# Kernel optimization log

Measured on AMD Instinct MI355X. Metric: run time of the kernel, lower is better.

## Reference

```python
import jax, jax.numpy as jnp
import numpy as np

ALPHA = 1.0  # self.alpha_ in ClusterNet


def setup_inputs() -> dict:
    key = jax.random.key(0)
    k1, k2 = jax.random.split(key)
    z = jax.random.normal(k1, (8192, 256), dtype=jnp.float32)
    centroids = jax.random.normal(k2, (64, 256), dtype=jnp.float32)
    return {"z": z, "centroids": centroids}


def reference(z, centroids):
    # similarity='EUC': pairwise euclidean distance (bs, n_clusters)
    diff = z[:, None, :] - centroids[None, :, :]          # (bs, K, H)
    sim = jnp.sqrt(jnp.sum(diff * diff, axis=2))          # (bs, K)
    # Student-t soft assignment, alpha = 1 -> Q = (1 + sim)^-1
    Q = jnp.power(1.0 + sim / ALPHA, -(ALPHA + 1.0) / 2.0)
    Q = Q / jnp.sum(Q, axis=1, keepdims=True)             # row-normalize
    # Target distribution P
    P = jnp.square(Q) / jnp.sum(Q, axis=0, keepdims=True)  # col-sum of Q
    P = P / jnp.sum(P, axis=1, keepdims=True)              # row-normalize
    return (Q, P)
```

## Files before the change

### kernel.cpp

```cpp
#include <hip/hip_runtime.h>


#define M  8192
#define NC 64
#define H  256
#define BM 64
#define BK 64
#define LDT 68

__global__ __launch_bounds__(256) void k1_dist_partial(
    const float* __restrict__ Z, const float* __restrict__ C,
    float* __restrict__ out)
{
    __shared__ float Zt[BK][LDT];
    __shared__ float Ct[BK][LDT];
    const int t  = threadIdx.x;
    const int bx = blockIdx.x;
    const int m0 = (bx >> 1) * BM;
    const int khalf = bx & 1;
    const int tx = t & 15, ty = t >> 4;
    const int kl = (t & 15) * 4;
    const int ml = t >> 4;

    float acc[4][4] = {};

    for (int chunk = 0; chunk < 2; ++chunk) {
        const int kb = khalf * 128 + chunk * BK;
        #pragma unroll
        for (int s = 0; s < 4; ++s) {
            const int m = ml + 16 * s;
            float4 v = *(const float4*)&Z[(m0 + m) * H + kb + kl];
            Zt[kl + 0][m] = v.x; Zt[kl + 1][m] = v.y;
            Zt[kl + 2][m] = v.z; Zt[kl + 3][m] = v.w;
            float4 w = *(const float4*)&C[m * H + kb + kl];
            Ct[kl + 0][m] = w.x; Ct[kl + 1][m] = w.y;
            Ct[kl + 2][m] = w.z; Ct[kl + 3][m] = w.w;
        }
        __syncthreads();
        #pragma unroll 8
        for (int kk = 0; kk < BK; ++kk) {
            float4 a4 = *(const float4*)&Zt[kk][ty * 4];
            float4 b4 = *(const float4*)&Ct[kk][tx * 4];
            float ar[4] = {a4.x, a4.y, a4.z, a4.w};
            float br[4] = {b4.x, b4.y, b4.z, b4.w};
            #pragma unroll
            for (int r = 0; r < 4; ++r)
                #pragma unroll
                for (int c = 0; c < 4; ++c) {
                    float d = ar[r] - br[c];
                    acc[r][c] += d * d;
                }
        }
        __syncthreads();
    }

    float* dst = out + (size_t)khalf * (M * NC);
    #pragma unroll
    for (int r = 0; r < 4; ++r) {
        float4 v = make_float4(acc[r][0], acc[r][1], acc[r][2], acc[r][3]);
        *(float4*)&dst[(m0 + ty * 4 + r) * NC + tx * 4] = v;
    }
}

__global__ void k0_zero(float* __restrict__ colsum) {
    colsum[threadIdx.x] = 0.0f;
}

__global__ __launch_bounds__(256) void k2_q(
    float* __restrict__ out, float* __restrict__ colsum)
{
    __shared__ float cs[NC];
    const int t = threadIdx.x;
    if (t < NC) cs[t] = 0.0f;
    __syncthreads();
    const int lane = t & 63;
    const int wid  = t >> 6;
    const int rowBase = blockIdx.x * 32;
    float local = 0.0f;
    for (int it = 0; it < 8; ++it) {
        const int row = rowBase + it * 4 + wid;
        float p0 = out[row * NC + lane];
        float p1 = out[(size_t)M * NC + row * NC + lane];
        float d  = sqrtf(p0 + p1);
        float q  = 1.0f / (1.0f + d);
        float s = q;
        #pragma unroll
        for (int m = 1; m < 64; m <<= 1) s += __shfl_xor(s, m);
        float Q = q / s;
        out[row * NC + lane] = Q;
        local += Q;
    }
    atomicAdd(&cs[lane], local);
    __syncthreads();
    if (t < NC) atomicAdd(&colsum[t], cs[t]);
}

__global__ __launch_bounds__(256) void k3_p(
    float* __restrict__ out, const float* __restrict__ colsum)
{
    const int t = threadIdx.x;
    const int lane = t & 63;
    const int wid  = t >> 6;
    const float invcs = 1.0f / colsum[lane];
    const int rowBase = blockIdx.x * 32;
    for (int it = 0; it < 8; ++it) {
        const int row = rowBase + it * 4 + wid;
        float q  = out[row * NC + lane];
        float pr = q * q * invcs;
        float s = pr;
        #pragma unroll
        for (int m = 1; m < 64; m <<= 1) s += __shfl_xor(s, m);
        out[(size_t)M * NC + row * NC + lane] = pr / s;
    }
}

extern "C" void kernel_launch(void* const* d_in, const int* in_sizes, int n_in,
                              void* d_out, int out_size, void* d_ws, size_t ws_size,
                              hipStream_t stream) {
    const float* Z = (const float*)d_in[0];
    const float* C = (const float*)d_in[1];
    float* out = (float*)d_out;
    float* colsum = (float*)d_ws;

    k0_zero<<<1, NC, 0, stream>>>(colsum);
    k1_dist_partial<<<256, 256, 0, stream>>>(Z, C, out);
    k2_q<<<256, 256, 0, stream>>>(out, colsum);
    k3_p<<<256, 256, 0, stream>>>(out, colsum);
}
```

Before: 89.91 us.

## Fuse distance and Q computation via norm expansion, drop atomics and extra launches

```diff
diff --git a/kernel.cpp b/kernel.cpp
--- a/kernel.cpp
+++ b/kernel.cpp
@@ -4,113 +4,149 @@
 #define M  8192
 #define NC 64
 #define H  256
-#define BM 64
-#define BK 64
-#define LDT 68
+#define BM 32
 
-__global__ __launch_bounds__(256) void k1_dist_partial(
+__global__ __launch_bounds__(256, 1) void k1_fused(
     const float* __restrict__ Z, const float* __restrict__ C,
-    float* __restrict__ out)
+    float* __restrict__ out, float* __restrict__ ws)
 {
-    __shared__ float Zt[BK][LDT];
-    __shared__ float Ct[BK][LDT];
-    const int t  = threadIdx.x;
-    const int bx = blockIdx.x;
-    const int m0 = (bx >> 1) * BM;
-    const int khalf = bx & 1;
-    const int tx = t & 15, ty = t >> 4;
-    const int kl = (t & 15) * 4;
-    const int ml = t >> 4;
+    __shared__ float pd[4][BM][NC];
+    __shared__ float ncp[4][NC];
+    __shared__ float nzs[BM];
+    __shared__ float csum[4][NC];
 
-    float acc[4][4] = {};
+    const int t    = threadIdx.x;
+    const int lane = t & 63;
+    const int wid  = __builtin_amdgcn_readfirstlane(t >> 6);
+    const int row0 = blockIdx.x * BM;
 
-    for (int chunk = 0; chunk < 2; ++chunk) {
-        const int kb = khalf * 128 + chunk * BK;
+    {
+        const int r  = t >> 3;
+        const int sg = t & 7;
+        const float4* zr = (const float4*)(Z + (size_t)(row0 + r) * H);
+        float s = 0.f;
         #pragma unroll
-        for (int s = 0; s < 4; ++s) {
-            const int m = ml + 16 * s;
-            float4 v = *(const float4*)&Z[(m0 + m) * H + kb + kl];
-            Zt[kl + 0][m] = v.x; Zt[kl + 1][m] = v.y;
-            Zt[kl + 2][m] = v.z; Zt[kl + 3][m] = v.w;
-            float4 w = *(const float4*)&C[m * H + kb + kl];
-            Ct[kl + 0][m] = w.x; Ct[kl + 1][m] = w.y;
-            Ct[kl + 2][m] = w.z; Ct[kl + 3][m] = w.w;
+        for (int i = 0; i < 8; ++i) {
+            float4 v = zr[sg * 8 + i];
+            s += v.x * v.x + v.y * v.y + v.z * v.z + v.w * v.w;
         }
-        __syncthreads();
-        #pragma unroll 8
-        for (int kk = 0; kk < BK; ++kk) {
-            float4 a4 = *(const float4*)&Zt[kk][ty * 4];
-            float4 b4 = *(const float4*)&Ct[kk][tx * 4];
-            float ar[4] = {a4.x, a4.y, a4.z, a4.w};
-            float br[4] = {b4.x, b4.y, b4.z, b4.w};
-            #pragma unroll
-            for (int r = 0; r < 4; ++r)
-                #pragma unroll
-                for (int c = 0; c < 4; ++c) {
-                    float d = ar[r] - br[c];
-                    acc[r][c] += d * d;
-                }
-        }
-        __syncthreads();
+        s += __shfl_xor(s, 1);
+        s += __shfl_xor(s, 2);
+        s += __shfl_xor(s, 4);
+        if (sg == 0) nzs[r] = s;
     }
 
-    float* dst = out + (size_t)khalf * (M * NC);
+    float4 c4[16];
+    {
+        const float4* cp = (const float4*)(C + (size_t)lane * H + wid * 64);
+        #pragma unroll
+        for (int i = 0; i < 16; ++i) c4[i] = cp[i];
+    }
+    {
+        float s = 0.f;
+        #pragma unroll
+        for (int i = 0; i < 16; ++i)
+            s += c4[i].x * c4[i].x + c4[i].y * c4[i].y + c4[i].z * c4[i].z + c4[i].w * c4[i].w;
+        ncp[wid][lane] = s;
+    }
+
+    float acc[BM];
     #pragma unroll
-    for (int r = 0; r < 4; ++r) {
-        float4 v = make_float4(acc[r][0], acc[r][1], acc[r][2], acc[r][3]);
-        *(float4*)&dst[(m0 + ty * 4 + r) * NC + tx * 4] = v;
+    for (int r = 0; r < BM; ++r) acc[r] = 0.f;
+
+    const float* Zb = Z + (size_t)row0 * H + wid * 64;
+    #pragma unroll
+    for (int kb = 0; kb < 4; ++kb) {
+        #pragma unroll
+        for (int r = 0; r < BM; ++r) {
+            const float4* zp = (const float4*)(Zb + r * H + kb * 16);
+            float4 z0 = zp[0], z1 = zp[1], z2 = zp[2], z3 = zp[3];
+            float a = acc[r];
+            a += z0.x * c4[kb*4+0].x + z0.y * c4[kb*4+0].y + z0.z * c4[kb*4+0].z + z0.w * c4[kb*4+0].w;
+            a += z1.x * c4[kb*4+1].x + z1.y * c4[kb*4+1].y + z1.z * c4[kb*4+1].z + z1.w * c4[kb*4+1].w;
+            a += z2.x * c4[kb*4+2].x + z2.y * c4[kb*4+2].y + z2.z * c4[kb*4+2].z + z2.w * c4[kb*4+2].w;
+            a += z3.x * c4[kb*4+3].x + z3.y * c4[kb*4+3].y + z3.z * c4[kb*4+3].z + z3.w * c4[kb*4+3].w;
+            acc[r] = a;
+        }
     }
+
+    #pragma unroll
+    for (int r = 0; r < BM; ++r) pd[wid][r][lane] = acc[r];
+    __syncthreads();
+
+    const float ncT = ncp[0][lane] + ncp[1][lane] + ncp[2][lane] + ncp[3][lane];
+    float colLocal = 0.f;
+    #pragma unroll
+    for (int j = 0; j < 8; ++j) {
+        const int r = wid * 8 + j;
+        float dot = pd[0][r][lane] + pd[1][r][lane] + pd[2][r][lane] + pd[3][r][lane];
+        float d2  = fmaxf(nzs[r] + ncT - 2.f * dot, 0.f);
+        float q   = 1.f / (1.f + sqrtf(d2));
+        float s = q;
+        s += __shfl_xor(s, 1);
+        s += __shfl_xor(s, 2);
+        s += __shfl_xor(s, 4);
+        s += __shfl_xor(s, 8);
+        s += __shfl_xor(s, 16);
+        s += __shfl_xor(s, 32);
+        float qn = q / s;
+        out[(size_t)(row0 + r) * NC + lane] = qn;
+        colLocal += qn;
+    }
+    csum[wid][lane] = colLocal;
+    __syncthreads();
+    if (wid == 0)
+        ws[blockIdx.x * NC + lane] =
+            csum[0][lane] + csum[1][lane] + csum[2][lane] + csum[3][lane];
 }
 
-__global__ void k0_zero(float* __restrict__ colsum) {
-    colsum[threadIdx.x] = 0.0f;
-}
+__global__ __launch_bounds__(256, 1) void k2_p(
+    float* __restrict__ out, const float* __restrict__ ws)
+{
+    __shared__ float4 red[256];
+    __shared__ float invcs[NC];
+    const int t  = threadIdx.x;
+    const int g  = t & 15;
+    const int s0 = t >> 4;
+    const float4* w4 = (const float4*)ws;
+    float4 a = make_float4(0.f, 0.f, 0.f, 0.f);
+    #pragma unroll
+    for (int i = 0; i < 16; ++i) {
+        float4 v = w4[(size_t)(s0 + 16 * i) * 16 + g];
+        a.x += v.x; a.y += v.y; a.z += v.z; a.w += v.w;
+    }
+    red[t] = a;
+    __syncthreads();
+    if (t < 16) {
+        float4 s = red[t];
+        for (int i = 1; i < 16; ++i) {
+            float4 v = red[i * 16 + t];
+            s.x += v.x; s.y += v.y; s.z += v.z; s.w += v.w;
+        }
+        invcs[4 * t + 0] = 1.f / s.x;
+        invcs[4 * t + 1] = 1.f / s.y;
+        invcs[4 * t + 2] = 1.f / s.z;
+        invcs[4 * t + 3] = 1.f / s.w;
+    }
+    __syncthreads();
 
-__global__ __launch_bounds__(256) void k2_q(
-    float* __restrict__ out, float* __restrict__ colsum)
-{
-    __shared__ float cs[NC];
-    const int t = threadIdx.x;
-    if (t < NC) cs[t] = 0.0f;
-    __syncthreads();
     const int lane = t & 63;
     const int wid  = t >> 6;
-    const int rowBase = blockIdx.x * 32;
-    float local = 0.0f;
-    for (int it = 0; it < 8; ++it) {
-        const int row = rowBase + it * 4 + wid;
-        float p0 = out[row * NC + lane];
-        float p1 = out[(size_t)M * NC + row * NC + lane];
-        float d  = sqrtf(p0 + p1);
-        float q  = 1.0f / (1.0f + d);
-        float s = q;
-        #pragma unroll
-        for (int m = 1; m < 64; m <<= 1) s += __shfl_xor(s, m);
-        float Q = q / s;
-        out[row * NC + lane] = Q;
-        local += Q;
-    }
-    atomicAdd(&cs[lane], local);
-    __syncthreads();
-    if (t < NC) atomicAdd(&colsum[t], cs[t]);
-}
-
-__global__ __launch_bounds__(256) void k3_p(
-    float* __restrict__ out, const float* __restrict__ colsum)
-{
-    const int t = threadIdx.x;
-    const int lane = t & 63;
-    const int wid  = t >> 6;
-    const float invcs = 1.0f / colsum[lane];
-    const int rowBase = blockIdx.x * 32;
-    for (int it = 0; it < 8; ++it) {
-        const int row = rowBase + it * 4 + wid;
-        float q  = out[row * NC + lane];
-        float pr = q * q * invcs;
+    const float ic = invcs[lane];
+    const int row0 = blockIdx.x * BM;
+    #pragma unroll
+    for (int j = 0; j < 8; ++j) {
+        const int r = row0 + wid * 8 + j;
+        float q  = out[(size_t)r * NC + lane];
+        float pr = q * q * ic;
         float s = pr;
-        #pragma unroll
-        for (int m = 1; m < 64; m <<= 1) s += __shfl_xor(s, m);
-        out[(size_t)M * NC + row * NC + lane] = pr / s;
+        s += __shfl_xor(s, 1);
+        s += __shfl_xor(s, 2);
+        s += __shfl_xor(s, 4);
+        s += __shfl_xor(s, 8);
+        s += __shfl_xor(s, 16);
+        s += __shfl_xor(s, 32);
+        out[(size_t)(M + r) * NC + lane] = pr / s;
     }
 }
 
@@ -120,10 +156,8 @@
     const float* Z = (const float*)d_in[0];
     const float* C = (const float*)d_in[1];
     float* out = (float*)d_out;
-    float* colsum = (float*)d_ws;
+    float* ws  = (float*)d_ws;
 
-    k0_zero<<<1, NC, 0, stream>>>(colsum);
-    k1_dist_partial<<<256, 256, 0, stream>>>(Z, C, out);
-    k2_q<<<256, 256, 0, stream>>>(out, colsum);
-    k3_p<<<256, 256, 0, stream>>>(out, colsum);
+    k1_fused<<<256, 256, 0, stream>>>(Z, C, out, ws);
+    k2_p<<<256, 256, 0, stream>>>(out, ws);
 }
```

Result: faster. 81.45 us (-9.4%).
